# Kernel tuning notes

Measured on AMD Instinct MI355X. Metric: run time of the kernel, lower is better.

Reference implementation:

```python
import jax, jax.numpy as jnp
import numpy as np

CONFUSED_PAIRS = [(1, 2), (3, 4), (5, 6)]
NUM_CLASSES = 13
MARGIN = 0.5
IGNORE_INDEX = -100
BIG = 1e9  # finite sentinel instead of +/-inf (keeps grads clean)
EPS = 1e-12  # matches F.normalize eps

_conf_np = np.zeros((NUM_CLASSES, NUM_CLASSES), dtype=bool)
for _a, _b in CONFUSED_PAIRS:
    _conf_np[_a, _b] = True
    _conf_np[_b, _a] = True
CONF = jnp.asarray(_conf_np)  # [C, C] symmetric confused-class table


def setup_inputs() -> dict:
    key = jax.random.key(0)
    k1, k2 = jax.random.split(key)
    embeddings = jax.random.normal(k1, (16, 512, 256), dtype=jnp.float32)
    labels = jax.random.randint(k2, (16, 512), 0, 13, dtype=jnp.int64)
    return {"embeddings": embeddings, "labels": labels}


def reference(embeddings, labels):
    B, S, H = embeddings.shape
    e = embeddings.reshape(-1, H)                      # [N, H]
    lab = labels.reshape(-1)                           # [N]
    N = e.shape[0]

    valid = lab != IGNORE_INDEX                        # [N]
    # L2 normalize (F.normalize: divide by norm clamped to eps)
    norm = jnp.linalg.norm(e, axis=1, keepdims=True)
    e = e / jnp.maximum(norm, EPS)

    sim = e @ e.T                                      # [N, N] cosine sims

    lab_c = jnp.clip(lab, 0, NUM_CLASSES - 1)          # safe gather index
    # anchor label participates in some confused pair, and anchor is valid
    anchor_ok = valid & CONF[lab_c].any(axis=1)        # [N]

    same = lab[:, None] == lab[None, :]                # [N, N]
    eye = jnp.eye(N, dtype=bool)
    pos_mask = same & valid[None, :] & ~eye            # positives: same class, not self
    neg_mask = CONF[lab_c[:, None], lab_c[None, :]] & valid[None, :]  # confused-class negatives

    has_pos = pos_mask.any(axis=1)
    has_neg = neg_mask.any(axis=1)
    count_mask = anchor_ok & has_pos & has_neg         # [N] anchors contributing a triplet

    hardest_pos = jnp.min(jnp.where(pos_mask, sim, BIG), axis=1)   # [N]
    hardest_neg = jnp.max(jnp.where(neg_mask, sim, -BIG), axis=1)  # [N]

    triplet = jax.nn.relu(MARGIN + hardest_neg - hardest_pos)
    triplet = jnp.where(count_mask, triplet, 0.0)

    num_triplets = count_mask.sum()
    loss = triplet.sum() / jnp.maximum(num_triplets, 1).astype(triplet.dtype)
    return jnp.where(num_triplets > 0, loss, 0.0)
```

## Files before the change

kernel.cpp:

```cpp
#include <hip/hip_runtime.h>
#include <math.h>

#define Hdim    256
#define NMAX    8192
#define NPADMAX (NMAX + 6 * 32)
#define WLMAX   264
#define BIGV    1e9f
#define MARGIN  0.5f

typedef __attribute__((ext_vector_type(8))) short bf16x8;
typedef __attribute__((ext_vector_type(4))) float f32x4;

struct WS {
    unsigned short ebf[NMAX][Hdim];
    int idx[NPADMAX];
    int S[8];
    int n[8];
    int wl_a[WLMAX];
    int wl_c[WLMAX];
    int T;
    unsigned done;
    float wsum;
    int   wcnt;
};

__device__ inline unsigned short f2bf(float f) {
    unsigned u = __float_as_uint(f);
    return (unsigned short)((u + 0x7fffu + ((u >> 16) & 1u)) >> 16);
}

__global__ __launch_bounds__(1024) void prep_kernel(const float* __restrict__ in,
                                                    const int* __restrict__ lab,
                                                    WS* ws, int N) {
    if (blockIdx.x == 0) {
        __shared__ int h[8], S[8], cur[8], ntp[8];
        const int tid = threadIdx.x;
        if (tid < 8) h[tid] = 0;
        __syncthreads();

        for (int i = tid; i < N; i += 1024) {
            int l = lab[i];
            if (l >= 1 && l <= 6) atomicAdd(&h[l], 1);
        }
        __syncthreads();

        if (tid == 0) {
            int acc = 0, tt = 0;
            #pragma unroll
            for (int c = 1; c <= 6; ++c) {
                S[c]   = acc; acc += ((h[c] + 31) >> 5) << 5;
                ntp[c] = tt;  tt  += (h[c] + 31) >> 5;
            }
            S[0] = 0; S[7] = acc; ntp[0] = 0; ntp[7] = tt;
            ws->T = tt;
            ws->done = 0u; ws->wsum = 0.f; ws->wcnt = 0;
            #pragma unroll
            for (int c = 0; c < 8; ++c) { ws->n[c] = h[c]; ws->S[c] = S[c]; }
        }
        __syncthreads();

        if (tid < 8) cur[tid] = S[tid];
        if (tid < ntp[7]) {
            int c = 1;
            while (tid >= ntp[c + 1]) ++c;
            ws->wl_a[tid] = S[c] + ((tid - ntp[c]) << 5);
            ws->wl_c[tid] = c;
        }
        if (tid < 192) {
            int c = (tid >> 5) + 1;
            int s = S[c] + h[c] + (tid & 31);
            if (s < S[c + 1]) ws->idx[s] = 0;
        }
        __syncthreads();

        for (int i = tid; i < N; i += 1024) {
            int l = lab[i];
            if (l >= 1 && l <= 6) ws->idx[atomicAdd(&cur[l], 1)] = i;
        }
    } else {
        const int row  = (blockIdx.x - 1) * 16 + (threadIdx.x >> 6);
        const int lane = threadIdx.x & 63;
        if (row >= N) return;
        const int l = lab[row];
        if (l < 1 || l > 6) return;
        float4 v = ((const float4*)(in + (size_t)row * Hdim))[lane];
        float ss = v.x*v.x + v.y*v.y + v.z*v.z + v.w*v.w;
        #pragma unroll
        for (int off = 32; off >= 1; off >>= 1) ss += __shfl_xor(ss, off);
        float sc = 1.0f / fmaxf(sqrtf(ss), 1e-12f);
        ushort4 o;
        o.x = f2bf(v.x * sc); o.y = f2bf(v.y * sc);
        o.z = f2bf(v.z * sc); o.w = f2bf(v.w * sc);
        ((ushort4*)(&ws->ebf[row][0]))[lane] = o;
    }
}

__global__ __launch_bounds__(256) void sim_kernel(WS* ws, float* __restrict__ out) {
    const int wave = threadIdx.x >> 6;
    const int lane = threadIdx.x & 63;
    const int col  = lane & 15;
    const int quad = lane >> 4;
    const int tileIdx = blockIdx.x;

    __shared__ float lds_hp[4][32], lds_hn[4][32];

    if (tileIdx < ws->T) {
        const int aBase = ws->wl_a[tileIdx];
        const int c     = ws->wl_c[tileIdx];
        const int p     = ((c - 1) ^ 1) + 1;
        const int posS = ws->S[c], posRealE = posS + ws->n[c];
        const int negS = ws->S[p], negRealE = negS + ws->n[p];
        const int nPosT = (ws->S[c + 1] - posS) >> 4;
        const int nNegT = (ws->S[p + 1] - negS) >> 4;
        const int nTT   = nPosT + nNegT;
        const bool hasPN = (ws->n[c] >= 2) && (ws->n[p] >= 1);

        const unsigned short* ebf = &ws->ebf[0][0];
        const int* __restrict__ idx = ws->idx;

        bf16x8 afrag[2][8];
        #pragma unroll
        for (int t2 = 0; t2 < 2; ++t2) {
            int ar = idx[aBase + t2 * 16 + col];
            const unsigned short* rp = ebf + (size_t)ar * Hdim + quad * 8;
            #pragma unroll
            for (int ks = 0; ks < 8; ++ks)
                afrag[t2][ks] = *(const bf16x8*)(rp + ks * 32);
        }

        float runMin[2][4], runMax[2][4];
        #pragma unroll
        for (int t2 = 0; t2 < 2; ++t2)
            #pragma unroll
            for (int r = 0; r < 4; ++r) { runMin[t2][r] = BIGV; runMax[t2][r] = -BIGV; }

        auto j0Of = [&](int t) -> int {
            return (t < nPosT) ? (posS + (t << 4)) : (negS + ((t - nPosT) << 4));
        };
        bf16x8 b0[8], b1[8];
        auto loadB = [&](bf16x8 (&bf)[8], int t) {
            int jr = idx[j0Of(t) + col];
            const unsigned short* rp = ebf + (size_t)jr * Hdim + quad * 8;
            #pragma unroll
            for (int ks = 0; ks < 8; ++ks)
                bf[ks] = *(const bf16x8*)(rp + ks * 32);
        };
        auto computeT = [&](bf16x8 (&bf)[8], int t) {
            int j0 = j0Of(t);
            bool isPos = t < nPosT;
            int realE  = isPos ? posRealE : negRealE;
            bool valid = (j0 + col) < realE;
            #pragma unroll
            for (int t2 = 0; t2 < 2; ++t2) {
                f32x4 acc = {0.f, 0.f, 0.f, 0.f};
                #pragma unroll
                for (int ks = 0; ks < 8; ++ks)
                    acc = __builtin_amdgcn_mfma_f32_16x16x32_bf16(afrag[t2][ks], bf[ks], acc, 0, 0, 0);
                if (isPos) {
                    #pragma unroll
                    for (int r = 0; r < 4; ++r)
                        runMin[t2][r] = fminf(runMin[t2][r], valid ? acc[r] : BIGV);
                } else {
                    #pragma unroll
                    for (int r = 0; r < 4; ++r)
                        runMax[t2][r] = fmaxf(runMax[t2][r], valid ? acc[r] : -BIGV);
                }
            }
        };

        int nIter = (nTT > wave) ? ((nTT - wave + 3) >> 2) : 0;
        int t = wave, i = 0;
        if (nIter > 0) loadB(b0, t);
        while (i + 2 <= nIter) {
            loadB(b1, t + 4);
            computeT(b0, t);
            if (i + 2 < nIter) loadB(b0, t + 8);
            computeT(b1, t + 4);
            t += 8; i += 2;
        }
        if (i < nIter) computeT(b0, t);

        #pragma unroll
        for (int t2 = 0; t2 < 2; ++t2)
            #pragma unroll
            for (int r = 0; r < 4; ++r) {
                float mn = runMin[t2][r], mx = runMax[t2][r];
                #pragma unroll
                for (int off = 1; off < 16; off <<= 1) {
                    mn = fminf(mn, __shfl_xor(mn, off));
                    mx = fmaxf(mx, __shfl_xor(mx, off));
                }
                if (col == 0) {
                    int a = t2 * 16 + quad * 4 + r;
                    lds_hp[wave][a] = mn;
                    lds_hn[wave][a] = mx;
                }
            }
        __syncthreads();

        if (wave == 0) {
            float contrib = 0.f; int cc = 0;
            if (lane < 32) {
                float hp = fminf(fminf(lds_hp[0][lane], lds_hp[1][lane]),
                                 fminf(lds_hp[2][lane], lds_hp[3][lane]));
                float hn = fmaxf(fmaxf(lds_hn[0][lane], lds_hn[1][lane]),
                                 fmaxf(lds_hn[2][lane], lds_hn[3][lane]));
                bool real = (aBase + lane) < posRealE;
                if (real && hasPN) {
                    float tr = MARGIN + hn - hp;
                    contrib = (tr > 0.f) ? tr : 0.f;
                    cc = 1;
                }
            }
            #pragma unroll
            for (int off = 32; off >= 1; off >>= 1) {
                contrib += __shfl_xor(contrib, off);
                cc      += __shfl_xor(cc, off);
            }
            if (lane == 0) {
                atomicAdd(&ws->wsum, contrib);
                atomicAdd(&ws->wcnt, cc);
            }
        }
    }

    if (threadIdx.x == 0) {
        __builtin_amdgcn_s_waitcnt(0);
        unsigned old = atomicAdd(&ws->done, 1u);
        if (old == (unsigned)(gridDim.x - 1)) {
            float s = atomicAdd(&ws->wsum, 0.0f);
            int   n = atomicAdd(&ws->wcnt, 0);
            out[0] = (n > 0) ? s / (float)n : 0.f;
        }
    }
}

extern "C" void kernel_launch(void* const* d_in, const int* in_sizes, int n_in,
                              void* d_out, int out_size, void* d_ws, size_t ws_size,
                              hipStream_t stream) {
    const float* emb = (const float*)d_in[0];
    const int*   lab = (const int*)d_in[1];
    int N = in_sizes[1];
    WS* ws = (WS*)d_ws;

    prep_kernel<<<1 + (N + 15) / 16, 1024, 0, stream>>>(emb, lab, ws, N);
    sim_kernel<<<WLMAX, 256, 0, stream>>>(ws, (float*)d_out);
}
```

Baseline: 94.58 us.

## Widen anchor tiles to 64 rows and replace atomic bucketing with ballot scan

Each sim block now holds 64 anchor rows in registers instead of 32. Every B tile loaded from global memory then feeds twice as many MFMAs, and the number of blocks roughly halves. The prep kernel replaces its LDS atomic histogram and atomic scatter with wave ballot/popcount counting and a deterministic per-wave prefix-offset scatter. The risks are higher register pressure, fewer blocks to spread across CUs, and more padding per class.

```diff
diff --git a/kernel.cpp b/kernel.cpp
--- a/kernel.cpp
+++ b/kernel.cpp
@@ -3,8 +3,9 @@
 
 #define Hdim    256
 #define NMAX    8192
-#define NPADMAX (NMAX + 6 * 32)
-#define WLMAX   264
+#define APAD    64
+#define NPADMAX (NMAX + 6 * APAD)
+#define WLMAX   144
 #define BIGV    1e9f
 #define MARGIN  0.5f
 
@@ -33,49 +34,79 @@
                                                     const int* __restrict__ lab,
                                                     WS* ws, int N) {
     if (blockIdx.x == 0) {
-        __shared__ int h[8], S[8], cur[8], ntp[8];
-        const int tid = threadIdx.x;
-        if (tid < 8) h[tid] = 0;
-        __syncthreads();
-
-        for (int i = tid; i < N; i += 1024) {
-            int l = lab[i];
-            if (l >= 1 && l <= 6) atomicAdd(&h[l], 1);
-        }
+        __shared__ int cnt[16][8];
+        __shared__ int off[16][8];
+        __shared__ int S[8], h[8], ntp[8];
+        const int tid  = threadIdx.x;
+        const int lane = tid & 63;
+        const int wv   = tid >> 6;
+
+        int l[8];
+        #pragma unroll
+        for (int k = 0; k < 8; ++k) {
+            int i = tid + (k << 10);
+            l[k] = (i < N) ? lab[i] : 0;
+        }
+
+        int cw[7] = {0, 0, 0, 0, 0, 0, 0};
+        #pragma unroll
+        for (int k = 0; k < 8; ++k)
+            #pragma unroll
+            for (int c = 1; c <= 6; ++c)
+                cw[c] += (int)__popcll(__ballot(l[k] == c));
+        if (lane == 0)
+            #pragma unroll
+            for (int c = 1; c <= 6; ++c) cnt[wv][c] = cw[c];
         __syncthreads();
 
         if (tid == 0) {
             int acc = 0, tt = 0;
-            #pragma unroll
             for (int c = 1; c <= 6; ++c) {
-                S[c]   = acc; acc += ((h[c] + 31) >> 5) << 5;
-                ntp[c] = tt;  tt  += (h[c] + 31) >> 5;
+                int hc = 0;
+                for (int w = 0; w < 16; ++w) hc += cnt[w][c];
+                h[c]   = hc;
+                S[c]   = acc; acc += ((hc + APAD - 1) / APAD) * APAD;
+                ntp[c] = tt;  tt  += (hc + APAD - 1) / APAD;
             }
             S[0] = 0; S[7] = acc; ntp[0] = 0; ntp[7] = tt;
             ws->T = tt;
             ws->done = 0u; ws->wsum = 0.f; ws->wcnt = 0;
-            #pragma unroll
-            for (int c = 0; c < 8; ++c) { ws->n[c] = h[c]; ws->S[c] = S[c]; }
+            ws->n[0] = 0; ws->n[7] = 0;
+            for (int c = 1; c <= 6; ++c) ws->n[c] = h[c];
+            for (int c = 0; c < 8; ++c) ws->S[c] = S[c];
+            for (int c = 1; c <= 6; ++c) {
+                int a = S[c];
+                for (int w = 0; w < 16; ++w) { off[w][c] = a; a += cnt[w][c]; }
+            }
         }
         __syncthreads();
 
-        if (tid < 8) cur[tid] = S[tid];
         if (tid < ntp[7]) {
             int c = 1;
             while (tid >= ntp[c + 1]) ++c;
-            ws->wl_a[tid] = S[c] + ((tid - ntp[c]) << 5);
+            ws->wl_a[tid] = S[c] + (tid - ntp[c]) * APAD;
             ws->wl_c[tid] = c;
         }
-        if (tid < 192) {
-            int c = (tid >> 5) + 1;
-            int s = S[c] + h[c] + (tid & 31);
+        if (tid < 6 * APAD) {
+            int c = (tid >> 6) + 1;
+            int s = S[c] + h[c] + (tid & 63);
             if (s < S[c + 1]) ws->idx[s] = 0;
         }
-        __syncthreads();
-
-        for (int i = tid; i < N; i += 1024) {
-            int l = lab[i];
-            if (l >= 1 && l <= 6) ws->idx[atomicAdd(&cur[l], 1)] = i;
+
+        int oc[7];
+        #pragma unroll
+        for (int c = 1; c <= 6; ++c) oc[c] = off[wv][c];
+        const unsigned long long below = (1ull << lane) - 1ull;
+        #pragma unroll
+        for (int k = 0; k < 8; ++k) {
+            int i = tid + (k << 10);
+            #pragma unroll
+            for (int c = 1; c <= 6; ++c) {
+                unsigned long long m = __ballot(l[k] == c);
+                if (l[k] == c)
+                    ws->idx[oc[c] + (int)__popcll(m & below)] = i;
+                oc[c] += (int)__popcll(m);
+            }
         }
     } else {
         const int row  = (blockIdx.x - 1) * 16 + (threadIdx.x >> 6);
@@ -86,7 +117,7 @@
         float4 v = ((const float4*)(in + (size_t)row * Hdim))[lane];
         float ss = v.x*v.x + v.y*v.y + v.z*v.z + v.w*v.w;
         #pragma unroll
-        for (int off = 32; off >= 1; off >>= 1) ss += __shfl_xor(ss, off);
+        for (int off2 = 32; off2 >= 1; off2 >>= 1) ss += __shfl_xor(ss, off2);
         float sc = 1.0f / fmaxf(sqrtf(ss), 1e-12f);
         ushort4 o;
         o.x = f2bf(v.x * sc); o.y = f2bf(v.y * sc);
@@ -102,7 +133,7 @@
     const int quad = lane >> 4;
     const int tileIdx = blockIdx.x;
 
-    __shared__ float lds_hp[4][32], lds_hn[4][32];
+    __shared__ float lds_hp[4][64], lds_hn[4][64];
 
     if (tileIdx < ws->T) {
         const int aBase = ws->wl_a[tileIdx];
@@ -118,21 +149,21 @@
         const unsigned short* ebf = &ws->ebf[0][0];
         const int* __restrict__ idx = ws->idx;
 
-        bf16x8 afrag[2][8];
-        #pragma unroll
-        for (int t2 = 0; t2 < 2; ++t2) {
-            int ar = idx[aBase + t2 * 16 + col];
+        bf16x8 afrag[4][8];
+        #pragma unroll
+        for (int g = 0; g < 4; ++g) {
+            int ar = idx[aBase + g * 16 + col];
             const unsigned short* rp = ebf + (size_t)ar * Hdim + quad * 8;
             #pragma unroll
             for (int ks = 0; ks < 8; ++ks)
-                afrag[t2][ks] = *(const bf16x8*)(rp + ks * 32);
-        }
-
-        float runMin[2][4], runMax[2][4];
-        #pragma unroll
-        for (int t2 = 0; t2 < 2; ++t2)
-            #pragma unroll
-            for (int r = 0; r < 4; ++r) { runMin[t2][r] = BIGV; runMax[t2][r] = -BIGV; }
+                afrag[g][ks] = *(const bf16x8*)(rp + ks * 32);
+        }
+
+        float runMin[4][4], runMax[4][4];
+        #pragma unroll
+        for (int g = 0; g < 4; ++g)
+            #pragma unroll
+            for (int r = 0; r < 4; ++r) { runMin[g][r] = BIGV; runMax[g][r] = -BIGV; }
 
         auto j0Of = [&](int t) -> int {
             return (t < nPosT) ? (posS + (t << 4)) : (negS + ((t - nPosT) << 4));
@@ -151,19 +182,19 @@
             int realE  = isPos ? posRealE : negRealE;
             bool valid = (j0 + col) < realE;
             #pragma unroll
-            for (int t2 = 0; t2 < 2; ++t2) {
+            for (int g = 0; g < 4; ++g) {
                 f32x4 acc = {0.f, 0.f, 0.f, 0.f};
                 #pragma unroll
                 for (int ks = 0; ks < 8; ++ks)
-                    acc = __builtin_amdgcn_mfma_f32_16x16x32_bf16(afrag[t2][ks], bf[ks], acc, 0, 0, 0);
+                    acc = __builtin_amdgcn_mfma_f32_16x16x32_bf16(afrag[g][ks], bf[ks], acc, 0, 0, 0);
                 if (isPos) {
                     #pragma unroll
                     for (int r = 0; r < 4; ++r)
-                        runMin[t2][r] = fminf(runMin[t2][r], valid ? acc[r] : BIGV);
+                        runMin[g][r] = fminf(runMin[g][r], valid ? acc[r] : BIGV);
                 } else {
                     #pragma unroll
                     for (int r = 0; r < 4; ++r)
-                        runMax[t2][r] = fmaxf(runMax[t2][r], valid ? acc[r] : -BIGV);
+                        runMax[g][r] = fmaxf(runMax[g][r], valid ? acc[r] : -BIGV);
                 }
             }
         };
@@ -181,17 +212,17 @@
         if (i < nIter) computeT(b0, t);
 
         #pragma unroll
-        for (int t2 = 0; t2 < 2; ++t2)
+        for (int g = 0; g < 4; ++g)
             #pragma unroll
             for (int r = 0; r < 4; ++r) {
-                float mn = runMin[t2][r], mx = runMax[t2][r];
+                float mn = runMin[g][r], mx = runMax[g][r];
                 #pragma unroll
                 for (int off = 1; off < 16; off <<= 1) {
                     mn = fminf(mn, __shfl_xor(mn, off));
                     mx = fmaxf(mx, __shfl_xor(mx, off));
                 }
                 if (col == 0) {
-                    int a = t2 * 16 + quad * 4 + r;
+                    int a = g * 16 + quad * 4 + r;
                     lds_hp[wave][a] = mn;
                     lds_hn[wave][a] = mx;
                 }
@@ -199,18 +230,16 @@
         __syncthreads();
 
         if (wave == 0) {
+            float hp = fminf(fminf(lds_hp[0][lane], lds_hp[1][lane]),
+                             fminf(lds_hp[2][lane], lds_hp[3][lane]));
+            float hn = fmaxf(fmaxf(lds_hn[0][lane], lds_hn[1][lane]),
+                             fmaxf(lds_hn[2][lane], lds_hn[3][lane]));
+            bool real = (aBase + lane) < posRealE;
             float contrib = 0.f; int cc = 0;
-            if (lane < 32) {
-                float hp = fminf(fminf(lds_hp[0][lane], lds_hp[1][lane]),
-                                 fminf(lds_hp[2][lane], lds_hp[3][lane]));
-                float hn = fmaxf(fmaxf(lds_hn[0][lane], lds_hn[1][lane]),
-                                 fmaxf(lds_hn[2][lane], lds_hn[3][lane]));
-                bool real = (aBase + lane) < posRealE;
-                if (real && hasPN) {
-                    float tr = MARGIN + hn - hp;
-                    contrib = (tr > 0.f) ? tr : 0.f;
-                    cc = 1;
-                }
+            if (real && hasPN) {
+                float tr = MARGIN + hn - hp;
+                contrib = (tr > 0.f) ? tr : 0.f;
+                cc = 1;
             }
             #pragma unroll
             for (int off = 32; off >= 1; off >>= 1) {
```

Measured after the change: 100.9 us. 1.07x slower.
